# Optimization experiments

Hardware: AMD Instinct MI355X
Metric: run time of the kernel (lower is better)

Reference implementation:

```python
import jax, jax.numpy as jnp
import numpy as np

HEAD_NUM = 8
DIM_QK = 64
DIM_V = 64
SPAN = 64
STRIDE = 4


def _sparse_indices(length_q, length_kv):
    # Replicates torch meshgrid index math (static, numpy).
    R = SPAN // STRIDE
    r = np.arange(R)[:, None]              # [R,1]
    c = np.arange(length_q)[None, :]       # [1,Lq]
    # ceil((c-(span-1))/stride) + r, via floor-div identity ceil(a/b) = -((-a)//b)
    qi_col = -((SPAN - 1 - c) // STRIDE) + r   # [R,Lq]
    qi_row = c - STRIDE * qi_col
    valid = (qi_row >= 0) & (qi_row < SPAN) & (qi_col >= 0) & (qi_col < length_kv)
    qc = np.clip(qi_col, 0, length_kv - 1)
    return jnp.asarray(qc, dtype=jnp.int32), jnp.asarray(valid)


def setup_inputs() -> dict:
    key = jax.random.key(0)
    ks = jax.random.split(key, 7)
    B, Lq, Lkv, D = 2, 4096, 1024, 512
    q = jax.random.normal(ks[0], (B, Lq, D), dtype=jnp.float32)
    k = jax.random.normal(ks[1], (B, Lkv, D), dtype=jnp.float32)
    v = jax.random.normal(ks[2], (B, Lkv, D), dtype=jnp.float32)
    Wq = jax.random.normal(ks[3], (D, HEAD_NUM * DIM_QK), dtype=jnp.float32) * 0.05
    Wk = jax.random.normal(ks[4], (D, HEAD_NUM * DIM_QK), dtype=jnp.float32) * 0.05
    Wv = jax.random.normal(ks[5], (D, HEAD_NUM * DIM_V), dtype=jnp.float32) * 0.05
    Wout = jax.random.normal(ks[6], (HEAD_NUM * DIM_V, D), dtype=jnp.float32) * 0.05
    return {"q": q, "k": k, "v": v, "Wq": Wq, "Wk": Wk, "Wv": Wv, "Wout": Wout}


def reference(q, k, v, Wq, Wk, Wv, Wout):
    B, Lq, _ = q.shape
    Lkv = k.shape[1]
    # Projections -> [B, H, L, D]
    Q = (q @ Wq).reshape(B, Lq, HEAD_NUM, DIM_QK).transpose(0, 2, 1, 3)
    K = (k @ Wk).reshape(B, Lkv, HEAD_NUM, DIM_QK).transpose(0, 2, 1, 3)
    V = (v @ Wv).reshape(B, Lkv, HEAD_NUM, DIM_V).transpose(0, 2, 1, 3)
    qc, valid = _sparse_indices(Lq, Lkv)          # [R,Lq]
    Kg = K[:, :, qc, :]                            # [B,H,R,Lq,DQK] gather
    scores = jnp.einsum("bhcd,bhrcd->bhrc", Q, Kg) / jnp.sqrt(jnp.float32(DIM_QK))
    big_neg = jnp.asarray(-1e30, scores.dtype)
    scores = jnp.where(valid[None, None], scores, big_neg)
    w = jax.nn.softmax(scores, axis=2)             # softmax over the R sparse slots
    w = jnp.where(valid[None, None], w, 0.0)
    Vg = V[:, :, qc, :]                            # [B,H,R,Lq,DV] gather
    ctx = jnp.einsum("bhrc,bhrcd->bhcd", w, Vg)   # [B,H,Lq,DV]
    ctx = ctx.transpose(0, 2, 1, 3).reshape(B, Lq, HEAD_NUM * DIM_V)
    return ctx @ Wout
```

## Files before the change

kernel.cpp:

```cpp
#include <hip/hip_runtime.h>
#include <math.h>

#define HN 8
#define DK 64
#define LQ 4096
#define LKV 1024
#define DMODEL 512
#define BATCH 2

typedef unsigned short u16;
typedef unsigned int u32;
typedef __attribute__((ext_vector_type(8))) __bf16 bf16x8;
typedef __attribute__((ext_vector_type(4))) float f32x4;
typedef __attribute__((ext_vector_type(8))) u16 u16x8;
typedef __attribute__((ext_vector_type(4))) u16 u16x4;

__device__ __forceinline__ u16 f2bf(float f) {
    u32 u = __float_as_uint(f);
    u = u + 0x7fffu + ((u >> 16) & 1u);
    return (u16)(u >> 16);
}

__device__ __forceinline__ void gl_lds16(const u16* g, u16* l) {
    __builtin_amdgcn_global_load_lds((const __attribute__((address_space(1))) u32*)g,
                                     (__attribute__((address_space(3))) u32*)l, 16, 0, 0);
}

__device__ __forceinline__ void gemm_body(const u16* __restrict__ A,
                                          const u16* __restrict__ Bt,
                                          float* __restrict__ C,
                                          int bx, int by) {
    __shared__ u16 As[128 * 32];
    __shared__ u16 Bs[128 * 32];

    const int tid = threadIdx.x;
    const int lane = tid & 63;
    const int wave = tid >> 6;
    const int wm = (wave >> 1) * 64;
    const int wn = (wave & 1) * 64;
    const int quad = lane >> 4;
    const int l16 = lane & 15;
    const size_t m0 = (size_t)by * 128;
    const size_t n0 = (size_t)bx * 128;

    f32x4 acc[4][4] = {};

    for (int k0 = 0; k0 < 512; k0 += 32) {
#pragma unroll
        for (int i = 0; i < 2; ++i) {
            const int id = i * 256 + tid;
            const int r = id >> 2;
            const int cs = id & 3;
            const int c = cs ^ ((r >> 1) & 3);
            const u16* ga = &A[(m0 + r) * 512 + k0 + c * 8];
            const u16* gb = &Bt[(n0 + r) * 512 + k0 + c * 8];
            u16* la = &As[(size_t)(i * 256 + wave * 64) * 8];
            u16* lb = &Bs[(size_t)(i * 256 + wave * 64) * 8];
            gl_lds16(ga, la);
            gl_lds16(gb, lb);
        }
        __syncthreads();

        bf16x8 af[4], bf[4];
#pragma unroll
        for (int i = 0; i < 4; ++i) {
            const int ra = wm + i * 16 + l16;
            const int ca = quad ^ ((ra >> 1) & 3);
            af[i] = *(const bf16x8*)&As[ra * 32 + ca * 8];
            const int rb = wn + i * 16 + l16;
            const int cb = quad ^ ((rb >> 1) & 3);
            bf[i] = *(const bf16x8*)&Bs[rb * 32 + cb * 8];
        }
#pragma unroll
        for (int i = 0; i < 4; ++i)
#pragma unroll
            for (int j = 0; j < 4; ++j)
                acc[i][j] = __builtin_amdgcn_mfma_f32_16x16x32_bf16(af[i], bf[j], acc[i][j], 0, 0, 0);
        __syncthreads();
    }

#pragma unroll
    for (int i = 0; i < 4; ++i) {
#pragma unroll
        for (int j = 0; j < 4; ++j) {
            const size_t row = m0 + wm + i * 16 + quad * 4;
            const size_t col = n0 + wn + j * 16 + l16;
#pragma unroll
            for (int t = 0; t < 4; ++t)
                C[(row + t) * 512 + col] = acc[i][j][t];
        }
    }
}

__global__ __launch_bounds__(256) void proj_fused(const u16* __restrict__ qb,
                                                  const u16* __restrict__ kb,
                                                  const u16* __restrict__ vb,
                                                  const u16* __restrict__ wqt,
                                                  const u16* __restrict__ wkt,
                                                  const u16* __restrict__ wvt,
                                                  float* __restrict__ Qf,
                                                  float* __restrict__ Kf,
                                                  float* __restrict__ Vf) {
    const int z = blockIdx.z;
    if (z > 0 && blockIdx.y >= 16) return;
    const u16* A = (z == 0) ? qb : (z == 1) ? kb : vb;
    const u16* Bt = (z == 0) ? wqt : (z == 1) ? wkt : wvt;
    float* C = (z == 0) ? Qf : (z == 1) ? Kf : Vf;
    gemm_body(A, Bt, C, blockIdx.x, blockIdx.y);
}

__global__ __launch_bounds__(256) void gemm_out(const u16* __restrict__ A,
                                                const u16* __restrict__ Bt,
                                                float* __restrict__ C) {
    gemm_body(A, Bt, C, blockIdx.x, blockIdx.y);
}

__global__ __launch_bounds__(256) void cvt_bf16(const float* __restrict__ in,
                                                u16* __restrict__ out, int n8) {
    const int i = blockIdx.x * 256 + threadIdx.x;
    if (i >= n8) return;
    const float4 a = ((const float4*)in)[i * 2];
    const float4 b = ((const float4*)in)[i * 2 + 1];
    u16x8 r;
    r[0] = f2bf(a.x); r[1] = f2bf(a.y); r[2] = f2bf(a.z); r[3] = f2bf(a.w);
    r[4] = f2bf(b.x); r[5] = f2bf(b.y); r[6] = f2bf(b.z); r[7] = f2bf(b.w);
    *(u16x8*)&out[(size_t)i * 8] = r;
}

__global__ __launch_bounds__(256) void wtrans(const float* __restrict__ W0,
                                              const float* __restrict__ W1,
                                              const float* __restrict__ W2,
                                              const float* __restrict__ W3,
                                              u16* __restrict__ O0, u16* __restrict__ O1,
                                              u16* __restrict__ O2, u16* __restrict__ O3) {
    const int z = blockIdx.z;
    const float* W = (z == 0) ? W0 : (z == 1) ? W1 : (z == 2) ? W2 : W3;
    u16* O = (z == 0) ? O0 : (z == 1) ? O1 : (z == 2) ? O2 : O3;

    __shared__ float t[32][33];
    const int tx = threadIdx.x;
    const int ty = threadIdx.y;
    const int x = blockIdx.x * 32 + tx;
    const int y0 = blockIdx.y * 32;
#pragma unroll
    for (int i = ty; i < 32; i += 8) t[i][tx] = W[(size_t)(y0 + i) * 512 + x];
    __syncthreads();
#pragma unroll
    for (int i = ty; i < 32; i += 8)
        O[(size_t)(blockIdx.x * 32 + i) * 512 + y0 + tx] = f2bf(t[tx][i]);
}

__global__ __launch_bounds__(256) void attn_f32(const float* __restrict__ Q,
                                                const float* __restrict__ K,
                                                const float* __restrict__ V,
                                                u16* __restrict__ ctx) {
    __shared__ float Ks[80][68];
    __shared__ float Vs[80][68];

    const int tid = threadIdx.x;
    const int c0 = blockIdx.x * 256;
    const int h = blockIdx.y;
    const int b = blockIdx.z;

    const int fd_c0 = (63 - c0) >> 2;
    const int win_lo = (fd_c0 < 0) ? -fd_c0 : 0;

    for (int i = tid; i < 80 * 16; i += 256) {
        int row = i >> 4;
        int d4 = i & 15;
        int col = win_lo + row;
        if (col < LKV) {
            size_t base = ((size_t)(b * LKV + col)) * DMODEL + h * DK + d4 * 4;
            *(float4*)&Ks[row][d4 * 4] = *(const float4*)&K[base];
            *(float4*)&Vs[row][d4 * 4] = *(const float4*)&V[base];
        }
    }
    __syncthreads();

    const int c = c0 + tid;
    const int fd = (63 - c) >> 2;

    float4 qv[16];
    const float* qp = &Q[((size_t)(b * LQ + c)) * DMODEL + h * DK];
#pragma unroll
    for (int i = 0; i < 16; ++i) qv[i] = *(const float4*)&qp[i * 4];

    float sc[16];
    float mx = -3.0e38f;
#pragma unroll
    for (int r = 0; r < 16; ++r) {
        int col = r - fd;
        if (col < 0) col = 0;
        const float* kr = &Ks[col - win_lo][0];
        float s = 0.f;
#pragma unroll
        for (int i = 0; i < 16; ++i) {
            float4 kv = *(const float4*)&kr[i * 4];
            s += qv[i].x * kv.x + qv[i].y * kv.y + qv[i].z * kv.z + qv[i].w * kv.w;
        }
        s *= 0.125f;
        sc[r] = (r >= fd) ? s : -1.0e30f;
        mx = fmaxf(mx, sc[r]);
    }

    float sum = 0.f;
#pragma unroll
    for (int r = 0; r < 16; ++r) {
        sc[r] = __expf(sc[r] - mx);
        sum += sc[r];
    }
    const float inv = 1.0f / sum;

    float acc[64];
#pragma unroll
    for (int i = 0; i < 64; ++i) acc[i] = 0.f;
#pragma unroll
    for (int r = 0; r < 16; ++r) {
        const float w = sc[r] * inv;
        int col = r - fd;
        if (col < 0) col = 0;
        const float* vr = &Vs[col - win_lo][0];
#pragma unroll
        for (int i = 0; i < 64; ++i) acc[i] = fmaf(w, vr[i], acc[i]);
    }

    u16* cp = &ctx[((size_t)(b * LQ + c)) * DMODEL + h * DK];
#pragma unroll
    for (int i = 0; i < 16; ++i) {
        u16x4 o;
        o[0] = f2bf(acc[i * 4 + 0]);
        o[1] = f2bf(acc[i * 4 + 1]);
        o[2] = f2bf(acc[i * 4 + 2]);
        o[3] = f2bf(acc[i * 4 + 3]);
        *(u16x4*)&cp[i * 4] = o;
    }
}

extern "C" void kernel_launch(void* const* d_in, const int* in_sizes, int n_in,
                              void* d_out, int out_size, void* d_ws, size_t ws_size,
                              hipStream_t stream) {
    const float* q    = (const float*)d_in[0];
    const float* k    = (const float*)d_in[1];
    const float* v    = (const float*)d_in[2];
    const float* Wq   = (const float*)d_in[3];
    const float* Wk   = (const float*)d_in[4];
    const float* Wv   = (const float*)d_in[5];
    const float* Wout = (const float*)d_in[6];
    float* out = (float*)d_out;

    const size_t NQ = (size_t)BATCH * LQ * DMODEL;
    const size_t NK = (size_t)BATCH * LKV * DMODEL;
    const size_t NW = (size_t)DMODEL * DMODEL;

    float* Qf = (float*)d_ws;
    float* Kf = Qf + NQ;
    float* Vf = Kf + NK;
    u16* qb  = (u16*)(Vf + NK);
    u16* kb  = qb + NQ;
    u16* vb  = kb + NK;
    u16* cb  = vb + NK;
    u16* wqt = cb + NQ;
    u16* wkt = wqt + NW;
    u16* wvt = wkt + NW;
    u16* wot = wvt + NW;

    cvt_bf16<<<dim3((unsigned)(NQ / 8 / 256)), dim3(256), 0, stream>>>(q, qb, (int)(NQ / 8));
    cvt_bf16<<<dim3((unsigned)(NK / 8 / 256)), dim3(256), 0, stream>>>(k, kb, (int)(NK / 8));
    cvt_bf16<<<dim3((unsigned)(NK / 8 / 256)), dim3(256), 0, stream>>>(v, vb, (int)(NK / 8));

    wtrans<<<dim3(16, 16, 4), dim3(32, 8), 0, stream>>>(Wq, Wk, Wv, Wout, wqt, wkt, wvt, wot);

    proj_fused<<<dim3(4, 64, 3), dim3(256), 0, stream>>>(qb, kb, vb, wqt, wkt, wvt, Qf, Kf, Vf);

    attn_f32<<<dim3(LQ / 256, HN, BATCH), dim3(256), 0, stream>>>(Qf, Kf, Vf, cb);

    gemm_out<<<dim3(4, 64), dim3(256), 0, stream>>>(cb, wot, out);
}
```

Before: 138.9 us.

## Store projections in bf16, merge prep kernels, compact projection grid

The projection GEMM now writes Q/K/V as bf16 instead of fp32, and the attention kernel reads bf16 and widens it to fp32 in registers and LDS. This halves the intermediate write and read traffic. The three conversion launches and the weight transpose are merged into one prep kernel. The projection grid is flattened so it no longer launches early-exit blocks. Rounding Q/K/V to bf16 adds some precision loss.

Result: faster. 128.3 us (-7.6%).

```diff
diff --git a/kernel.cpp b/kernel.cpp
--- a/kernel.cpp
+++ b/kernel.cpp
@@ -13,22 +13,25 @@
 typedef __attribute__((ext_vector_type(8))) __bf16 bf16x8;
 typedef __attribute__((ext_vector_type(4))) float f32x4;
 typedef __attribute__((ext_vector_type(8))) u16 u16x8;
-typedef __attribute__((ext_vector_type(4))) u16 u16x4;
 
 __device__ __forceinline__ u16 f2bf(float f) {
     u32 u = __float_as_uint(f);
     u = u + 0x7fffu + ((u >> 16) & 1u);
     return (u16)(u >> 16);
 }
+__device__ __forceinline__ float bf2f(u16 u) {
+    return __uint_as_float(((u32)u) << 16);
+}
 
 __device__ __forceinline__ void gl_lds16(const u16* g, u16* l) {
     __builtin_amdgcn_global_load_lds((const __attribute__((address_space(1))) u32*)g,
                                      (__attribute__((address_space(3))) u32*)l, 16, 0, 0);
 }
 
+template <bool BF16OUT>
 __device__ __forceinline__ void gemm_body(const u16* __restrict__ A,
                                           const u16* __restrict__ Bt,
-                                          float* __restrict__ C,
+                                          void* __restrict__ Cp,
                                           int bx, int by) {
     __shared__ u16 As[128 * 32];
     __shared__ u16 Bs[128 * 32];
@@ -86,8 +89,12 @@
             const size_t row = m0 + wm + i * 16 + quad * 4;
             const size_t col = n0 + wn + j * 16 + l16;
 #pragma unroll
-            for (int t = 0; t < 4; ++t)
-                C[(row + t) * 512 + col] = acc[i][j][t];
+            for (int t = 0; t < 4; ++t) {
+                if (BF16OUT)
+                    ((u16*)Cp)[(row + t) * 512 + col] = f2bf(acc[i][j][t]);
+                else
+                    ((float*)Cp)[(row + t) * 512 + col] = acc[i][j][t];
+            }
         }
     }
 }
@@ -98,61 +105,74 @@
                                                   const u16* __restrict__ wqt,
                                                   const u16* __restrict__ wkt,
                                                   const u16* __restrict__ wvt,
-                                                  float* __restrict__ Qf,
-                                                  float* __restrict__ Kf,
-                                                  float* __restrict__ Vf) {
-    const int z = blockIdx.z;
-    if (z > 0 && blockIdx.y >= 16) return;
-    const u16* A = (z == 0) ? qb : (z == 1) ? kb : vb;
-    const u16* Bt = (z == 0) ? wqt : (z == 1) ? wkt : wvt;
-    float* C = (z == 0) ? Qf : (z == 1) ? Kf : Vf;
-    gemm_body(A, Bt, C, blockIdx.x, blockIdx.y);
+                                                  u16* __restrict__ Qb,
+                                                  u16* __restrict__ Kb,
+                                                  u16* __restrict__ Vb) {
+    const int idx = blockIdx.x;
+    if (idx < 256)
+        gemm_body<true>(qb, wqt, Qb, idx & 3, idx >> 2);
+    else if (idx < 320)
+        gemm_body<true>(kb, wkt, Kb, (idx - 256) & 3, (idx - 256) >> 2);
+    else
+        gemm_body<true>(vb, wvt, Vb, (idx - 320) & 3, (idx - 320) >> 2);
 }
 
 __global__ __launch_bounds__(256) void gemm_out(const u16* __restrict__ A,
                                                 const u16* __restrict__ Bt,
                                                 float* __restrict__ C) {
-    gemm_body(A, Bt, C, blockIdx.x, blockIdx.y);
-}
-
-__global__ __launch_bounds__(256) void cvt_bf16(const float* __restrict__ in,
-                                                u16* __restrict__ out, int n8) {
-    const int i = blockIdx.x * 256 + threadIdx.x;
-    if (i >= n8) return;
-    const float4 a = ((const float4*)in)[i * 2];
-    const float4 b = ((const float4*)in)[i * 2 + 1];
-    u16x8 r;
-    r[0] = f2bf(a.x); r[1] = f2bf(a.y); r[2] = f2bf(a.z); r[3] = f2bf(a.w);
-    r[4] = f2bf(b.x); r[5] = f2bf(b.y); r[6] = f2bf(b.z); r[7] = f2bf(b.w);
-    *(u16x8*)&out[(size_t)i * 8] = r;
-}
-
-__global__ __launch_bounds__(256) void wtrans(const float* __restrict__ W0,
-                                              const float* __restrict__ W1,
-                                              const float* __restrict__ W2,
-                                              const float* __restrict__ W3,
-                                              u16* __restrict__ O0, u16* __restrict__ O1,
-                                              u16* __restrict__ O2, u16* __restrict__ O3) {
-    const int z = blockIdx.z;
-    const float* W = (z == 0) ? W0 : (z == 1) ? W1 : (z == 2) ? W2 : W3;
-    u16* O = (z == 0) ? O0 : (z == 1) ? O1 : (z == 2) ? O2 : O3;
-
-    __shared__ float t[32][33];
-    const int tx = threadIdx.x;
-    const int ty = threadIdx.y;
-    const int x = blockIdx.x * 32 + tx;
-    const int y0 = blockIdx.y * 32;
-#pragma unroll
-    for (int i = ty; i < 32; i += 8) t[i][tx] = W[(size_t)(y0 + i) * 512 + x];
-    __syncthreads();
-#pragma unroll
-    for (int i = ty; i < 32; i += 8)
-        O[(size_t)(blockIdx.x * 32 + i) * 512 + y0 + tx] = f2bf(t[tx][i]);
-}
-
-__global__ __launch_bounds__(256) void attn_f32(const float* __restrict__ Q,
-                                                const float* __restrict__ K,
-                                                const float* __restrict__ V,
+    gemm_body<false>(A, Bt, C, blockIdx.x & 3, blockIdx.x >> 2);
+}
+
+__global__ __launch_bounds__(256) void prep(const float* __restrict__ q,
+                                            const float* __restrict__ k,
+                                            const float* __restrict__ v,
+                                            const float* __restrict__ Wq,
+                                            const float* __restrict__ Wk,
+                                            const float* __restrict__ Wv,
+                                            const float* __restrict__ Wout,
+                                            u16* __restrict__ qb, u16* __restrict__ kb,
+                                            u16* __restrict__ vb,
+                                            u16* __restrict__ wqt, u16* __restrict__ wkt,
+                                            u16* __restrict__ wvt, u16* __restrict__ wot) {
+    __shared__ float tbuf[32][33];
+    const int bid = blockIdx.x;
+    const int tid = threadIdx.x;
+
+    if (bid < 3072) {
+        const float* in;
+        u16* outp;
+        int i;
+        if (bid < 2048)      { in = q; outp = qb; i = bid * 256 + tid; }
+        else if (bid < 2560) { in = k; outp = kb; i = (bid - 2048) * 256 + tid; }
+        else                 { in = v; outp = vb; i = (bid - 2560) * 256 + tid; }
+        const float4 a = ((const float4*)in)[i * 2];
+        const float4 b = ((const float4*)in)[i * 2 + 1];
+        u16x8 r;
+        r[0] = f2bf(a.x); r[1] = f2bf(a.y); r[2] = f2bf(a.z); r[3] = f2bf(a.w);
+        r[4] = f2bf(b.x); r[5] = f2bf(b.y); r[6] = f2bf(b.z); r[7] = f2bf(b.w);
+        *(u16x8*)&outp[(size_t)i * 8] = r;
+    } else {
+        const int wb = bid - 3072;
+        const int z = wb >> 8;
+        const int t = wb & 255;
+        const float* W = (z == 0) ? Wq : (z == 1) ? Wk : (z == 2) ? Wv : Wout;
+        u16* O = (z == 0) ? wqt : (z == 1) ? wkt : (z == 2) ? wvt : wot;
+        const int tx = tid & 31;
+        const int ty = tid >> 5;
+        const int x = (t & 15) * 32 + tx;
+        const int y0 = (t >> 4) * 32;
+#pragma unroll
+        for (int i = ty; i < 32; i += 8) tbuf[i][tx] = W[(size_t)(y0 + i) * 512 + x];
+        __syncthreads();
+#pragma unroll
+        for (int i = ty; i < 32; i += 8)
+            O[(size_t)((t & 15) * 32 + i) * 512 + y0 + tx] = f2bf(tbuf[tx][i]);
+    }
+}
+
+__global__ __launch_bounds__(256) void attn_f32(const u16* __restrict__ Q,
+                                                const u16* __restrict__ K,
+                                                const u16* __restrict__ V,
                                                 u16* __restrict__ ctx) {
     __shared__ float Ks[80][68];
     __shared__ float Vs[80][68];
@@ -165,14 +185,22 @@
     const int fd_c0 = (63 - c0) >> 2;
     const int win_lo = (fd_c0 < 0) ? -fd_c0 : 0;
 
-    for (int i = tid; i < 80 * 16; i += 256) {
-        int row = i >> 4;
-        int d4 = i & 15;
+    for (int i = tid; i < 80 * 8; i += 256) {
+        int row = i >> 3;
+        int d8 = i & 7;
         int col = win_lo + row;
         if (col < LKV) {
-            size_t base = ((size_t)(b * LKV + col)) * DMODEL + h * DK + d4 * 4;
-            *(float4*)&Ks[row][d4 * 4] = *(const float4*)&K[base];
-            *(float4*)&Vs[row][d4 * 4] = *(const float4*)&V[base];
+            size_t base = ((size_t)(b * LKV + col)) * DMODEL + h * DK + d8 * 8;
+            u16x8 k8 = *(const u16x8*)&K[base];
+            u16x8 v8 = *(const u16x8*)&V[base];
+            float4 ka = make_float4(bf2f(k8[0]), bf2f(k8[1]), bf2f(k8[2]), bf2f(k8[3]));
+            float4 kb4 = make_float4(bf2f(k8[4]), bf2f(k8[5]), bf2f(k8[6]), bf2f(k8[7]));
+            float4 va = make_float4(bf2f(v8[0]), bf2f(v8[1]), bf2f(v8[2]), bf2f(v8[3]));
+            float4 vb4 = make_float4(bf2f(v8[4]), bf2f(v8[5]), bf2f(v8[6]), bf2f(v8[7]));
+            *(float4*)&Ks[row][d8 * 8] = ka;
+            *(float4*)&Ks[row][d8 * 8 + 4] = kb4;
+            *(float4*)&Vs[row][d8 * 8] = va;
+            *(float4*)&Vs[row][d8 * 8 + 4] = vb4;
         }
     }
     __syncthreads();
@@ -180,10 +208,14 @@
     const int c = c0 + tid;
     const int fd = (63 - c) >> 2;
 
-    float4 qv[16];
-    const float* qp = &Q[((size_t)(b * LQ + c)) * DMODEL + h * DK];
-#pragma unroll
-    for (int i = 0; i < 16; ++i) qv[i] = *(const float4*)&qp[i * 4];
+    float qreg[64];
+    const u16* qp = &Q[((size_t)(b * LQ + c)) * DMODEL + h * DK];
+#pragma unroll
+    for (int i = 0; i < 8; ++i) {
+        u16x8 t8 = *(const u16x8*)&qp[i * 8];
+#pragma unroll
+        for (int j = 0; j < 8; ++j) qreg[i * 8 + j] = bf2f(t8[j]);
+    }
 
     float sc[16];
     float mx = -3.0e38f;
@@ -194,10 +226,7 @@
         const float* kr = &Ks[col - win_lo][0];
         float s = 0.f;
 #pragma unroll
-        for (int i = 0; i < 16; ++i) {
-            float4 kv = *(const float4*)&kr[i * 4];
-            s += qv[i].x * kv.x + qv[i].y * kv.y + qv[i].z * kv.z + qv[i].w * kv.w;
-        }
+        for (int i = 0; i < 64; ++i) s = fmaf(qreg[i], kr[i], s);
         s *= 0.125f;
         sc[r] = (r >= fd) ? s : -1.0e30f;
         mx = fmaxf(mx, sc[r]);
@@ -226,13 +255,11 @@
 
     u16* cp = &ctx[((size_t)(b * LQ + c)) * DMODEL + h * DK];
 #pragma unroll
-    for (int i = 0; i < 16; ++i) {
-        u16x4 o;
-        o[0] = f2bf(acc[i * 4 + 0]);
-        o[1] = f2bf(acc[i * 4 + 1]);
-        o[2] = f2bf(acc[i * 4 + 2]);
-        o[3] = f2bf(acc[i * 4 + 3]);
-        *(u16x4*)&cp[i * 4] = o;
+    for (int i = 0; i < 8; ++i) {
+        u16x8 o;
+#pragma unroll
+        for (int j = 0; j < 8; ++j) o[j] = f2bf(acc[i * 8 + j]);
+        *(u16x8*)&cp[i * 8] = o;
     }
 }
 
@@ -252,27 +279,24 @@
     const size_t NK = (size_t)BATCH * LKV * DMODEL;
     const size_t NW = (size_t)DMODEL * DMODEL;
 
-    float* Qf = (float*)d_ws;
-    float* Kf = Qf + NQ;
-    float* Vf = Kf + NK;
-    u16* qb  = (u16*)(Vf + NK);
+    u16* qb  = (u16*)d_ws;
     u16* kb  = qb + NQ;
     u16* vb  = kb + NK;
-    u16* cb  = vb + NK;
+    u16* Qb  = vb + NK;
+    u16* Kb  = Qb + NQ;
+    u16* Vb  = Kb + NK;
+    u16* cb  = Vb + NK;
     u16* wqt = cb + NQ;
     u16* wkt = wqt + NW;
     u16* wvt = wkt + NW;
     u16* wot = wvt + NW;
 
-    cvt_bf16<<<dim3((unsigned)(NQ / 8 / 256)), dim3(256), 0, stream>>>(q, qb, (int)(NQ / 8));
-    cvt_bf16<<<dim3((unsigned)(NK / 8 / 256)), dim3(256), 0, stream>>>(k, kb, (int)(NK / 8));
-    cvt_bf16<<<dim3((unsigned)(NK / 8 / 256)), dim3(256), 0, stream>>>(v, vb, (int)(NK / 8));
-
-    wtrans<<<dim3(16, 16, 4), dim3(32, 8), 0, stream>>>(Wq, Wk, Wv, Wout, wqt, wkt, wvt, wot);
-
-    proj_fused<<<dim3(4, 64, 3), dim3(256), 0, stream>>>(qb, kb, vb, wqt, wkt, wvt, Qf, Kf, Vf);
-
-    attn_f32<<<dim3(LQ / 256, HN, BATCH), dim3(256), 0, stream>>>(Qf, Kf, Vf, cb);
-
-    gemm_out<<<dim3(4, 64), dim3(256), 0, stream>>>(cb, wot, out);
-}
+    prep<<<dim3(4096), dim3(256), 0, stream>>>(q, k, v, Wq, Wk, Wv, Wout,
+                                               qb, kb, vb, wqt, wkt, wvt, wot);
+
+    proj_fused<<<dim3(384), dim3(256), 0, stream>>>(qb, kb, vb, wqt, wkt, wvt, Qb, Kb, Vb);
+
+    attn_f32<<<dim3(LQ / 256, HN, BATCH), dim3(256), 0, stream>>>(Qb, Kb, Vb, cb);
+
+    gemm_out<<<dim3(256), dim3(256), 0, stream>>>(cb, wot, out);
+}
```
